# Kernel tuning notes

Measured on AMD Instinct MI355X. Metric: run time of the kernel, lower is better.

The kernel has to match this reference:

```python
import jax, jax.numpy as jnp
import numpy as np


def setup_inputs() -> dict:
    key = jax.random.key(0)
    k1, k2 = jax.random.split(key)
    S, D = 8192, 2048
    context_enc = jax.random.normal(k1, (S, D), dtype=jnp.float32)
    # nn.Linear(2D, D): W [D, 2D] stored as [out, in]; here kept as [D, 2D]
    W = jax.random.normal(k2, (D, 2 * D), dtype=jnp.float32) * (1.0 / np.sqrt(2 * D))
    b = jnp.zeros((D,), dtype=jnp.float32)
    return {"context_enc": context_enc, "W": W, "b": b}


def reference(context_enc, W, b):
    # Training path of HistoryCompression with mode='max-reset', window=None:
    #   history_compression = cummax(context_enc, dim=0)
    #   then sequential gated reset: state = hc[t] * sigmoid(Linear([state; ctx[t]]))
    D = context_enc.shape[1]
    hc = jax.lax.cummax(context_enc, axis=0)  # [S, D]
    # split W into the part acting on state and on ctx (avoids per-step concat)
    W_state, W_ctx = W[:, :D], W[:, D:]  # each [D, D]
    ctx_proj = context_enc @ W_ctx.T + b  # [S, D], precomputed (ctx part is static)
    init_state = jnp.full((D,), -1.0, dtype=context_enc.dtype)

    def step(state, inp):
        hc_t, ctx_proj_t = inp
        gate = jax.nn.sigmoid(state @ W_state.T + ctx_proj_t)
        new_state = hc_t * gate
        return new_state, new_state

    final_state, reset_history = jax.lax.scan(step, init_state, (hc, ctx_proj))
    return reset_history, final_state
```

## Files before the change

### kernel.cpp

```cpp
#include <hip/hip_runtime.h>
#include <stdint.h>

#define S_LEN 8192
#define DIM   2048
#define W2    4096

typedef __attribute__((ext_vector_type(8))) __bf16 bf16x8;
typedef __attribute__((ext_vector_type(4))) float  floatx4;
typedef __attribute__((ext_vector_type(2))) float  f32x2;
typedef unsigned long long u64;
typedef unsigned int       u32;

__global__ void init_pairs(u64* __restrict__ pairs) {
  int i = blockIdx.x * 256 + threadIdx.x;
  if (i < 2 * DIM) {
    pairs[i] = ((u64)__float_as_uint(-1.0f) << 32) | 0ull;
  }
}

__device__ inline bf16x8 pack_bf8(float4 a, float4 b) {
  bf16x8 h;
  h[0] = (__bf16)a.x; h[1] = (__bf16)a.y; h[2] = (__bf16)a.z; h[3] = (__bf16)a.w;
  h[4] = (__bf16)b.x; h[5] = (__bf16)b.y; h[6] = (__bf16)b.z; h[7] = (__bf16)b.w;
  return h;
}

__global__ __launch_bounds__(256) void gemm_ctx(const float* __restrict__ A,
                                                const float* __restrict__ W,
                                                const float* __restrict__ bias,
                                                float* __restrict__ C) {
  __shared__ __bf16 As[64][72];
  __shared__ __bf16 Bs[64][72];
  const int tid  = threadIdx.x;
  const int m0   = blockIdx.y * 64;
  const int n0   = blockIdx.x * 64;
  const int w    = tid >> 6;
  const int lane = tid & 63;
  const int wm   = w >> 1, wn = w & 1;
  const int r    = tid >> 2;
  const int seg  = tid & 3;

  floatx4 acc[2][2] = {};

  for (int k0 = 0; k0 < DIM; k0 += 64) {
    {
      const float* pa = A + (size_t)(m0 + r) * DIM + k0 + seg * 16;
      const float* pb = W + (size_t)(n0 + r) * W2 + DIM + k0 + seg * 16;
      float4 a0 = ((const float4*)pa)[0], a1 = ((const float4*)pa)[1];
      float4 a2 = ((const float4*)pa)[2], a3 = ((const float4*)pa)[3];
      float4 b0 = ((const float4*)pb)[0], b1 = ((const float4*)pb)[1];
      float4 b2 = ((const float4*)pb)[2], b3 = ((const float4*)pb)[3];
      *(bf16x8*)&As[r][seg * 16]     = pack_bf8(a0, a1);
      *(bf16x8*)&As[r][seg * 16 + 8] = pack_bf8(a2, a3);
      *(bf16x8*)&Bs[r][seg * 16]     = pack_bf8(b0, b1);
      *(bf16x8*)&Bs[r][seg * 16 + 8] = pack_bf8(b2, b3);
    }
    __syncthreads();
    #pragma unroll
    for (int kk = 0; kk < 64; kk += 32) {
      const int ks = kk + (lane >> 4) * 8;
      bf16x8 af[2], bfr[2];
      af[0]  = *(const bf16x8*)&As[32 * wm +      (lane & 15)][ks];
      af[1]  = *(const bf16x8*)&As[32 * wm + 16 + (lane & 15)][ks];
      bfr[0] = *(const bf16x8*)&Bs[32 * wn +      (lane & 15)][ks];
      bfr[1] = *(const bf16x8*)&Bs[32 * wn + 16 + (lane & 15)][ks];
      #pragma unroll
      for (int im = 0; im < 2; ++im)
        #pragma unroll
        for (int in = 0; in < 2; ++in)
          acc[im][in] = __builtin_amdgcn_mfma_f32_16x16x32_bf16(
              af[im], bfr[in], acc[im][in], 0, 0, 0);
    }
    __syncthreads();
  }

  #pragma unroll
  for (int in = 0; in < 2; ++in) {
    const int col = n0 + 32 * wn + 16 * in + (lane & 15);
    const float bv = bias[col];
    #pragma unroll
    for (int im = 0; im < 2; ++im) {
      const int rbase = m0 + 32 * wm + 16 * im + (lane >> 4) * 4;
      #pragma unroll
      for (int q = 0; q < 4; ++q)
        C[(size_t)(rbase + q) * DIM + col] = acc[im][in][q] + bv;
    }
  }
}

__global__ __launch_bounds__(512, 1) void recur(const float* __restrict__ W,
                                                const float* __restrict__ ce,
                                                float* __restrict__ out,
                                                u64* __restrict__ pairs) {
  __shared__ __align__(16) float st[2][DIM];
  const int tid = threadIdx.x;
  const int w = tid >> 6, l = tid & 63;
  const int i0 = blockIdx.x * 32;

  f32x2 w2[4][16];
  #pragma unroll
  for (int r2 = 0; r2 < 4; ++r2) {
    const float* wp = W + (size_t)(i0 + 4 * w + r2) * W2 + 32 * l;
    #pragma unroll
    for (int j = 0; j < 8; ++j) {
      float4 v = ((const float4*)wp)[j];
      w2[r2][2 * j + 0] = (f32x2){v.x, v.y};
      w2[r2][2 * j + 1] = (f32x2){v.z, v.w};
    }
  }

  const int rmap  = ((l & 1) << 1) | ((l >> 1) & 1);
  const int myrow = i0 + 4 * w + rmap;
  const bool owner = (l < 4);
  float hcm = -3.0e38f;
  float s_last = 0.f;
  u64* b0 = pairs;
  u64* b1 = pairs + DIM;
  const int base = tid * 4;
  const int slot4 = (4 * tid) ^ (((tid >> 3) & 7) << 2);

  float cev = 0.f, cxv = 0.f;
  if (owner) {
    cev = ce[myrow];
    cxv = out[myrow];
  }

  for (int t = 1; t <= S_LEN; ++t) {
    u64* src = ((t - 1) & 1) ? b1 : b0;
    const u32 want = (u32)(t - 1);
    u64 v[4];
    #pragma unroll
    for (int q = 0; q < 4; ++q)
      v[q] = __hip_atomic_load(&src[base + q], __ATOMIC_RELAXED,
                               __HIP_MEMORY_SCOPE_AGENT);
    for (;;) {
      u32 bad = 0;
      #pragma unroll
      for (int q = 0; q < 4; ++q)
        bad |= ((u32)v[q] != want) ? (1u << q) : 0u;
      if (!bad) break;
      #pragma unroll
      for (int q = 0; q < 4; ++q)
        if ((bad >> q) & 1u)
          v[q] = __hip_atomic_load(&src[base + q], __ATOMIC_RELAXED,
                                   __HIP_MEMORY_SCOPE_AGENT);
    }

    float ncev = 0.f, ncxv = 0.f;
    if (owner && t < S_LEN) {
      ncev = ce[(size_t)t * DIM + myrow];
      ncxv = out[(size_t)t * DIM + myrow];
    }

    float* stw = st[t & 1];
    {
      float4 sv4;
      sv4.x = __uint_as_float((u32)(v[0] >> 32));
      sv4.y = __uint_as_float((u32)(v[1] >> 32));
      sv4.z = __uint_as_float((u32)(v[2] >> 32));
      sv4.w = __uint_as_float((u32)(v[3] >> 32));
      *(float4*)&stw[slot4] = sv4;
    }
    asm volatile("s_waitcnt lgkmcnt(0)\n\ts_barrier" ::: "memory");

    f32x2 acc2[4] = {};
    #pragma unroll
    for (int jj = 0; jj < 8; ++jj) {
      const float4 sv = *(const float4*)&stw[32 * l + 4 * (jj ^ (l & 7))];
      const f32x2 s01 = (f32x2){sv.x, sv.y};
      const f32x2 s23 = (f32x2){sv.z, sv.w};
      #pragma unroll
      for (int r2 = 0; r2 < 4; ++r2) {
        acc2[r2] += w2[r2][2 * jj + 0] * s01;
        acc2[r2] += w2[r2][2 * jj + 1] * s23;
      }
    }
    float a0 = acc2[0].x + acc2[0].y;
    float a1 = acc2[1].x + acc2[1].y;
    float a2 = acc2[2].x + acc2[2].y;
    float a3 = acc2[3].x + acc2[3].y;

    float u0 = (l & 1) ? a0 : a2;
    float u1 = (l & 1) ? a1 : a3;
    float x0 = __shfl_xor(u0, 1, 64);
    float x1 = __shfl_xor(u1, 1, 64);
    float c0 = ((l & 1) ? a2 : a0) + x0;
    float c1 = ((l & 1) ? a3 : a1) + x1;
    float uu = (l & 2) ? c0 : c1;
    float xx = __shfl_xor(uu, 2, 64);
    float d  = ((l & 2) ? c1 : c0) + xx;
    #pragma unroll
    for (int m = 4; m < 64; m <<= 1) d += __shfl_xor(d, m, 64);

    if (owner) {
      float y = d + cxv;
      hcm = fmaxf(hcm, cev);
      float e = __expf(-y);
      float s = hcm * __builtin_amdgcn_rcpf(1.0f + e);
      u64* dst = (t & 1) ? b1 : b0;
      u64 pk = ((u64)__float_as_uint(s) << 32) | (u64)(u32)t;
      __hip_atomic_store(&dst[myrow], pk, __ATOMIC_RELAXED,
                         __HIP_MEMORY_SCOPE_AGENT);
      asm volatile("" ::: "memory");
      out[(size_t)(t - 1) * DIM + myrow] = s;
      s_last = s;
    }
    cev = ncev;
    cxv = ncxv;
  }

  if (owner) out[(size_t)S_LEN * DIM + myrow] = s_last;
}

extern "C" void kernel_launch(void* const* d_in, const int* in_sizes, int n_in,
                              void* d_out, int out_size, void* d_ws, size_t ws_size,
                              hipStream_t stream) {
  const float* ce = (const float*)d_in[0];
  const float* W  = (const float*)d_in[1];
  const float* b  = (const float*)d_in[2];
  float* out = (float*)d_out;
  u64* pairs = (u64*)d_ws;

  hipLaunchKernelGGL(init_pairs, dim3(16), dim3(256), 0, stream, pairs);
  hipLaunchKernelGGL(gemm_ctx, dim3(DIM / 64, S_LEN / 64), dim3(256), 0, stream,
                     ce, W, b, out);
  hipLaunchKernelGGL(recur, dim3(64), dim3(512), 0, stream, W, ce, out, pairs);
}
```

Measured before the change: 15.93 ms.

## Double recurrence block threads, halve rows per wave, use DPP reductions

The recurrent kernel now runs 1024 threads per block, so each wave handles 2 output rows instead of 4. Each thread holds half as many weight registers and polls 2 state pairs instead of 4, with a new LDS swizzle for the float2 state writes. The cross-lane reduction now combines the two rows with a 32-lane shuffle, then finishes with DPP row operations instead of a shuffle ladder. This aims to shorten the per-step dependent latency, at the cost of a 16-wave barrier per step and more polling traffic.

Measured after the change: 16.42 ms. 1.03x slower.

```diff
diff --git a/kernel.cpp b/kernel.cpp
--- a/kernel.cpp
+++ b/kernel.cpp
@@ -88,19 +88,25 @@
   }
 }
 
-__global__ __launch_bounds__(512, 1) void recur(const float* __restrict__ W,
-                                                const float* __restrict__ ce,
-                                                float* __restrict__ out,
-                                                u64* __restrict__ pairs) {
+template <int CTRL>
+__device__ __forceinline__ float dpp_add(float x) {
+  int s = __builtin_amdgcn_update_dpp(0, __float_as_int(x), CTRL, 0xF, 0xF, true);
+  return x + __int_as_float(s);
+}
+
+__global__ __launch_bounds__(1024, 1) void recur(const float* __restrict__ W,
+                                                 const float* __restrict__ ce,
+                                                 float* __restrict__ out,
+                                                 u64* __restrict__ pairs) {
   __shared__ __align__(16) float st[2][DIM];
   const int tid = threadIdx.x;
   const int w = tid >> 6, l = tid & 63;
   const int i0 = blockIdx.x * 32;
 
-  f32x2 w2[4][16];
+  f32x2 w2[2][16];
   #pragma unroll
-  for (int r2 = 0; r2 < 4; ++r2) {
-    const float* wp = W + (size_t)(i0 + 4 * w + r2) * W2 + 32 * l;
+  for (int r2 = 0; r2 < 2; ++r2) {
+    const float* wp = W + (size_t)(i0 + 2 * w + r2) * W2 + 32 * l;
     #pragma unroll
     for (int j = 0; j < 8; ++j) {
       float4 v = ((const float4*)wp)[j];
@@ -109,15 +115,15 @@
     }
   }
 
-  const int rmap  = ((l & 1) << 1) | ((l >> 1) & 1);
-  const int myrow = i0 + 4 * w + rmap;
-  const bool owner = (l < 4);
+  const int myrow = i0 + 2 * w + (l >> 5);
+  const bool owner = ((l & 31) == 0);
   float hcm = -3.0e38f;
   float s_last = 0.f;
   u64* b0 = pairs;
   u64* b1 = pairs + DIM;
-  const int base = tid * 4;
-  const int slot4 = (4 * tid) ^ (((tid >> 3) & 7) << 2);
+  const int base = tid * 2;
+  const int Fp    = (tid >> 1) ^ ((tid >> 4) & 7);
+  const int slot2 = 4 * Fp + 2 * (tid & 1);
 
   float cev = 0.f, cxv = 0.f;
   if (owner) {
@@ -128,22 +134,17 @@
   for (int t = 1; t <= S_LEN; ++t) {
     u64* src = ((t - 1) & 1) ? b1 : b0;
     const u32 want = (u32)(t - 1);
-    u64 v[4];
-    #pragma unroll
-    for (int q = 0; q < 4; ++q)
-      v[q] = __hip_atomic_load(&src[base + q], __ATOMIC_RELAXED,
-                               __HIP_MEMORY_SCOPE_AGENT);
-    for (;;) {
-      u32 bad = 0;
-      #pragma unroll
-      for (int q = 0; q < 4; ++q)
-        bad |= ((u32)v[q] != want) ? (1u << q) : 0u;
-      if (!bad) break;
-      #pragma unroll
-      for (int q = 0; q < 4; ++q)
-        if ((bad >> q) & 1u)
-          v[q] = __hip_atomic_load(&src[base + q], __ATOMIC_RELAXED,
-                                   __HIP_MEMORY_SCOPE_AGENT);
+    u64 v0 = __hip_atomic_load(&src[base + 0], __ATOMIC_RELAXED,
+                               __HIP_MEMORY_SCOPE_AGENT);
+    u64 v1 = __hip_atomic_load(&src[base + 1], __ATOMIC_RELAXED,
+                               __HIP_MEMORY_SCOPE_AGENT);
+    while (!(((u32)v0 == want) & ((u32)v1 == want))) {
+      if ((u32)v0 != want)
+        v0 = __hip_atomic_load(&src[base + 0], __ATOMIC_RELAXED,
+                               __HIP_MEMORY_SCOPE_AGENT);
+      if ((u32)v1 != want)
+        v1 = __hip_atomic_load(&src[base + 1], __ATOMIC_RELAXED,
+                               __HIP_MEMORY_SCOPE_AGENT);
     }
 
     float ncev = 0.f, ncxv = 0.f;
@@ -154,46 +155,38 @@
 
     float* stw = st[t & 1];
     {
-      float4 sv4;
-      sv4.x = __uint_as_float((u32)(v[0] >> 32));
-      sv4.y = __uint_as_float((u32)(v[1] >> 32));
-      sv4.z = __uint_as_float((u32)(v[2] >> 32));
-      sv4.w = __uint_as_float((u32)(v[3] >> 32));
-      *(float4*)&stw[slot4] = sv4;
+      float2 sv2;
+      sv2.x = __uint_as_float((u32)(v0 >> 32));
+      sv2.y = __uint_as_float((u32)(v1 >> 32));
+      *(float2*)&stw[slot2] = sv2;
     }
     asm volatile("s_waitcnt lgkmcnt(0)\n\ts_barrier" ::: "memory");
 
-    f32x2 acc2[4] = {};
+    f32x2 a0 = {}, a1 = {};
     #pragma unroll
     for (int jj = 0; jj < 8; ++jj) {
       const float4 sv = *(const float4*)&stw[32 * l + 4 * (jj ^ (l & 7))];
       const f32x2 s01 = (f32x2){sv.x, sv.y};
       const f32x2 s23 = (f32x2){sv.z, sv.w};
-      #pragma unroll
-      for (int r2 = 0; r2 < 4; ++r2) {
-        acc2[r2] += w2[r2][2 * jj + 0] * s01;
-        acc2[r2] += w2[r2][2 * jj + 1] * s23;
-      }
-    }
-    float a0 = acc2[0].x + acc2[0].y;
-    float a1 = acc2[1].x + acc2[1].y;
-    float a2 = acc2[2].x + acc2[2].y;
-    float a3 = acc2[3].x + acc2[3].y;
-
-    float u0 = (l & 1) ? a0 : a2;
-    float u1 = (l & 1) ? a1 : a3;
-    float x0 = __shfl_xor(u0, 1, 64);
-    float x1 = __shfl_xor(u1, 1, 64);
-    float c0 = ((l & 1) ? a2 : a0) + x0;
-    float c1 = ((l & 1) ? a3 : a1) + x1;
-    float uu = (l & 2) ? c0 : c1;
-    float xx = __shfl_xor(uu, 2, 64);
-    float d  = ((l & 2) ? c1 : c0) + xx;
-    #pragma unroll
-    for (int m = 4; m < 64; m <<= 1) d += __shfl_xor(d, m, 64);
+      a0 += w2[0][2 * jj + 0] * s01;
+      a0 += w2[0][2 * jj + 1] * s23;
+      a1 += w2[1][2 * jj + 0] * s01;
+      a1 += w2[1][2 * jj + 1] * s23;
+    }
+    float p0 = a0.x + a0.y;
+    float p1 = a1.x + a1.y;
+
+    float send = (l & 32) ? p0 : p1;
+    float got  = __shfl_xor(send, 32, 64);
+    float b    = ((l & 32) ? p1 : p0) + got;
+    b += __shfl_xor(b, 16, 64);
+    b = dpp_add<0xB1>(b);
+    b = dpp_add<0x4E>(b);
+    b = dpp_add<0x141>(b);
+    b = dpp_add<0x140>(b);
 
     if (owner) {
-      float y = d + cxv;
+      float y = b + cxv;
       hcm = fmaxf(hcm, cev);
       float e = __expf(-y);
       float s = hcm * __builtin_amdgcn_rcpf(1.0f + e);
@@ -224,5 +217,5 @@
   hipLaunchKernelGGL(init_pairs, dim3(16), dim3(256), 0, stream, pairs);
   hipLaunchKernelGGL(gemm_ctx, dim3(DIM / 64, S_LEN / 64), dim3(256), 0, stream,
                      ce, W, b, out);
-  hipLaunchKernelGGL(recur, dim3(64), dim3(512), 0, stream, W, ce, out, pairs);
-}
+  hipLaunchKernelGGL(recur, dim3(64), dim3(1024), 0, stream, W, ce, out, pairs);
+}
```
